# Performance work log

Hardware: AMD Instinct MI355X
Metric: run time of the kernel (lower is better)

The kernel has to match this reference:

```python
import jax, jax.numpy as jnp
import numpy as np

# Network topology constants (topological order: inputs, L hidden layers, outputs)
N_IN = 512
H = 1024      # hidden nodes per layer
L = 8         # hidden layers
N_OUT = 256
DEG = 64      # enabled incoming connections per non-input node
B = 1024      # batch of input vectors

LAYER_SIZES = [H] * L + [N_OUT]
E_TOTAL = sum(n * DEG for n in LAYER_SIZES)  # 540672


def setup_inputs() -> dict:
    key = jax.random.key(0)
    k_in, k_w = jax.random.split(key)
    inputs = jax.random.normal(k_in, (B, N_IN), dtype=jnp.float32)
    # scale weights ~1/sqrt(DEG) so sigmoid pre-activations are well-conditioned
    weights = jax.random.normal(k_w, (E_TOTAL,), dtype=jnp.float32) / np.sqrt(DEG)
    # src indices: for each layer, incoming edges may come from ANY earlier node
    rng = np.random.default_rng(0)
    src_chunks = []
    n_before = N_IN
    for n in LAYER_SIZES:
        src_chunks.append(rng.integers(0, n_before, size=n * DEG))
        n_before += n
    src_idx = jnp.asarray(np.concatenate(src_chunks), dtype=jnp.int32)
    return {"inputs": inputs, "weights": weights, "src_idx": src_idx}


def reference(inputs, weights, src_idx):
    # outs: [B, n_nodes_evaluated_so_far], grown layer by layer (topological order)
    outs = inputs
    off = 0
    for n in LAYER_SIZES:
        e = n * DEG
        s = src_idx[off:off + e]            # [e] gather indices into earlier nodes
        w = weights[off:off + e]            # [e]
        gathered = outs[:, s] * w           # [B, e] irregular gather + scale
        z = gathered.reshape(-1, n, DEG).sum(-1)  # per-node sum over DEG in-edges
        outs = jnp.concatenate([outs, jax.nn.sigmoid(z)], axis=1)
        off += e
    return outs[:, -N_OUT:]  # [B, N_OUT] outputs of 'output' nodes
```

## Files before the change

kernel.cpp:

```cpp
#include <hip/hip_runtime.h>
#include <math.h>


#define N_IN    512
#define NLAYER  9
#define DEG     64
#define BATCH   1024
#define BPB     4
#define THREADS 1024
#define TOTAL_N 8960
#define N_OUT   256
#define NGROUP  132

union H4 { uint2 u; _Float16 h[4]; };
union H2 { unsigned u; _Float16 h[2]; };
union HS { _Float16 h; unsigned short s; };

__global__ __launch_bounds__(256)
void neat_prep(const float* __restrict__ wts,
               const int*   __restrict__ sidx,
               uint4*       __restrict__ rec)
{
    __shared__ unsigned short srec[64 * 17 * 8];

    const int tid  = threadIdx.x;
    const int g    = blockIdx.x;
    const int wave = tid >> 6;
    const int lane = tid & 63;
    const unsigned long long lt = (1ull << lane) - 1ull;

    #pragma unroll 2
    for (int k = 0; k < 16; ++k) {
        const int l = (wave << 4) + k;
        const int j = (g << 12) + (l << 6) + lane;
        const int idx = sidx[j];
        HS w; w.h = (_Float16)wts[j];

        const int c = idx & 15;
        int start = 0, rank = 0;
        #pragma unroll
        for (int cc = 0; cc < 16; ++cc) {
            const unsigned long long m = __ballot(c == cc);
            if (cc < c)       start += (int)__popcll(m);
            else if (cc == c) rank   = (int)__popcll(m & lt);
        }

        const int sigma = ((l & 15) << 2) | (l >> 4);
        const int slot  = ((start + rank) - sigma) & 63;
        const int q = slot >> 2, gg = slot & 3;
        srec[((l * 17 + q) << 3) + gg]     = (unsigned short)idx;
        srec[((l * 17 + q) << 3) + 4 + gg] = w.s;
    }
    __syncthreads();

    const uint4* sr = reinterpret_cast<const uint4*>(srec);
    for (int r = tid; r < 1024; r += 256) {
        const int q = r >> 6, l = r & 63;
        rec[(g << 10) + r] = sr[l * 17 + q];
    }
}

__global__ __launch_bounds__(THREADS, 4)
void neat_fwd(const float* __restrict__ in,
              const uint4* __restrict__ rec,
              float*       __restrict__ out)
{
    __shared__ _Float16 act[TOTAL_N * BPB];

    const int tid   = threadIdx.x;
    const int bbase = blockIdx.x * BPB;

    {
        const float* src = in + bbase * N_IN;
        for (int t = tid; t < BPB * N_IN; t += THREADS) {
            int j = t >> 9;
            int i = t & (N_IN - 1);
            act[i * BPB + j] = (_Float16)src[t];
        }
    }
    __syncthreads();

    int recBase = 0;
    int nb      = N_IN;
    #pragma unroll 1
    for (int layer = 0; layer < NLAYER; ++layer) {
        const int n = (layer < NLAYER - 1) ? 1024 : N_OUT;
        if (tid < n) {
            const int neuron = tid;
            const uint4* rp = rec + recBase + ((neuron >> 6) << 10) + (neuron & 63);

            uint4 r[16];
            #pragma unroll
            for (int q = 0; q < 16; ++q) r[q] = rp[q << 6];

            float4 acc = make_float4(0.f, 0.f, 0.f, 0.f);
            #pragma unroll
            for (int q = 0; q < 16; ++q) {
                const uint4 r4 = r[q];
                H4 g0, g1, g2, g3;
                g0.u = *reinterpret_cast<const uint2*>(act + ((r4.x & 0xffffu) << 2));
                g1.u = *reinterpret_cast<const uint2*>(act + ((r4.x >> 16) << 2));
                g2.u = *reinterpret_cast<const uint2*>(act + ((r4.y & 0xffffu) << 2));
                g3.u = *reinterpret_cast<const uint2*>(act + ((r4.y >> 16) << 2));
                H2 wz, ww; wz.u = r4.z; ww.u = r4.w;
                acc.x += (float)g0.h[0] * (float)wz.h[0];
                acc.y += (float)g0.h[1] * (float)wz.h[0];
                acc.z += (float)g0.h[2] * (float)wz.h[0];
                acc.w += (float)g0.h[3] * (float)wz.h[0];
                acc.x += (float)g1.h[0] * (float)wz.h[1];
                acc.y += (float)g1.h[1] * (float)wz.h[1];
                acc.z += (float)g1.h[2] * (float)wz.h[1];
                acc.w += (float)g1.h[3] * (float)wz.h[1];
                acc.x += (float)g2.h[0] * (float)ww.h[0];
                acc.y += (float)g2.h[1] * (float)ww.h[0];
                acc.z += (float)g2.h[2] * (float)ww.h[0];
                acc.w += (float)g2.h[3] * (float)ww.h[0];
                acc.x += (float)g3.h[0] * (float)ww.h[1];
                acc.y += (float)g3.h[1] * (float)ww.h[1];
                acc.z += (float)g3.h[2] * (float)ww.h[1];
                acc.w += (float)g3.h[3] * (float)ww.h[1];
            }

            float4 sg;
            sg.x = 1.f / (1.f + __expf(-acc.x));
            sg.y = 1.f / (1.f + __expf(-acc.y));
            sg.z = 1.f / (1.f + __expf(-acc.z));
            sg.w = 1.f / (1.f + __expf(-acc.w));

            if (layer < NLAYER - 1) {
                H4 p;
                p.h[0] = (_Float16)sg.x; p.h[1] = (_Float16)sg.y;
                p.h[2] = (_Float16)sg.z; p.h[3] = (_Float16)sg.w;
                *reinterpret_cast<uint2*>(act + ((nb + neuron) << 2)) = p.u;
            } else {
                float* op = out + neuron;
                op[(bbase + 0) * N_OUT] = sg.x;
                op[(bbase + 1) * N_OUT] = sg.y;
                op[(bbase + 2) * N_OUT] = sg.z;
                op[(bbase + 3) * N_OUT] = sg.w;
            }
        }
        __syncthreads();
        recBase += n << 4;
        nb      += n;
    }
}

extern "C" void kernel_launch(void* const* d_in, const int* in_sizes, int n_in,
                              void* d_out, int out_size, void* d_ws, size_t ws_size,
                              hipStream_t stream)
{
    const float* in  = (const float*)d_in[0];
    const float* wts = (const float*)d_in[1];
    const int*   sx  = (const int*)d_in[2];
    float*       out = (float*)d_out;
    uint4*       rec = (uint4*)d_ws;

    neat_prep<<<NGROUP, 256, 0, stream>>>(wts, sx, rec);
    neat_fwd<<<BATCH / BPB, THREADS, 0, stream>>>(in, rec, out);
}
```

Measured before the change: 55.33 us.

## Fuse edge-record prep into forward kernel with a grid-wide barrier

Merges the separate prep kernel into the forward kernel. Every block first builds its share of the per-edge records with a new slot assignment that sorts by index bank and fills overflow into holes, then all blocks wait on a global atomic-flag barrier before running the layer loop. The aim is to remove the second kernel launch and the serial gap between the two kernels, and to spread prep across all 256 blocks. The cost is a hipMemsetAsync on the flag, two __syncthreads per prep iteration, and a spin barrier that only works if all 256 blocks are resident at the same time.

```diff
diff --git a/kernel.cpp b/kernel.cpp
--- a/kernel.cpp
+++ b/kernel.cpp
@@ -10,64 +10,28 @@
 #define THREADS 1024
 #define TOTAL_N 8960
 #define N_OUT   256
-#define NGROUP  132
+#define NEDGE_N 8448
+#define GRID    256
+#define PREPW   (GRID * 16)
 
 union H4 { uint2 u; _Float16 h[4]; };
 union H2 { unsigned u; _Float16 h[2]; };
 union HS { _Float16 h; unsigned short s; };
 
-__global__ __launch_bounds__(256)
-void neat_prep(const float* __restrict__ wts,
-               const int*   __restrict__ sidx,
-               uint4*       __restrict__ rec)
-{
-    __shared__ unsigned short srec[64 * 17 * 8];
-
-    const int tid  = threadIdx.x;
-    const int g    = blockIdx.x;
-    const int wave = tid >> 6;
-    const int lane = tid & 63;
-    const unsigned long long lt = (1ull << lane) - 1ull;
-
-    #pragma unroll 2
-    for (int k = 0; k < 16; ++k) {
-        const int l = (wave << 4) + k;
-        const int j = (g << 12) + (l << 6) + lane;
-        const int idx = sidx[j];
-        HS w; w.h = (_Float16)wts[j];
-
-        const int c = idx & 15;
-        int start = 0, rank = 0;
-        #pragma unroll
-        for (int cc = 0; cc < 16; ++cc) {
-            const unsigned long long m = __ballot(c == cc);
-            if (cc < c)       start += (int)__popcll(m);
-            else if (cc == c) rank   = (int)__popcll(m & lt);
-        }
-
-        const int sigma = ((l & 15) << 2) | (l >> 4);
-        const int slot  = ((start + rank) - sigma) & 63;
-        const int q = slot >> 2, gg = slot & 3;
-        srec[((l * 17 + q) << 3) + gg]     = (unsigned short)idx;
-        srec[((l * 17 + q) << 3) + 4 + gg] = w.s;
-    }
-    __syncthreads();
-
-    const uint4* sr = reinterpret_cast<const uint4*>(srec);
-    for (int r = tid; r < 1024; r += 256) {
-        const int q = r >> 6, l = r & 63;
-        rec[(g << 10) + r] = sr[l * 17 + q];
-    }
-}
-
 __global__ __launch_bounds__(THREADS, 4)
-void neat_fwd(const float* __restrict__ in,
-              const uint4* __restrict__ rec,
-              float*       __restrict__ out)
+void neat_fused(const float* __restrict__ in,
+                const float* __restrict__ wts,
+                const int*   __restrict__ sidx,
+                uint4*       __restrict__ rec,
+                int*         __restrict__ flag,
+                float*       __restrict__ out)
 {
     __shared__ _Float16 act[TOTAL_N * BPB];
+    __shared__ unsigned sortbuf[16][64];
 
     const int tid   = threadIdx.x;
+    const int wave  = tid >> 6;
+    const int lane  = tid & 63;
     const int bbase = blockIdx.x * BPB;
 
     {
@@ -78,7 +42,69 @@
             act[i * BPB + j] = (_Float16)src[t];
         }
     }
+
+    const unsigned long long lt = (1ull << lane) - 1ull;
+    const int wgid = blockIdx.x * 16 + wave;
+    for (int t = wgid; t < NEDGE_N; t += PREPW) {
+        const int e   = (t << 6) + lane;
+        const int idx = sidx[e];
+        HS w; w.h = (_Float16)wts[e];
+        const int c = idx & 15;
+
+        int rank = 0, spillbefore = 0;
+        #pragma unroll
+        for (int cc = 0; cc < 16; ++cc) {
+            const unsigned long long m = __ballot(c == cc);
+            const int n = (int)__popcll(m);
+            if (cc == c) rank = (int)__popcll(m & lt);
+            spillbefore += (cc < c && n > 4) ? (n - 4) : 0;
+        }
+        const bool spill = (rank >= 4);
+        int slot_pre = spill ? -1 : ((c << 2) + rank);
+        const int myspill = spillbefore + rank - 4;
+
+        int hcum = 0;
+        #pragma unroll
+        for (int cc = 0; cc < 16; ++cc) {
+            const unsigned long long m = __ballot(c == cc);
+            const int n = (int)__popcll(m);
+            int holes = 4 - n; holes = holes > 0 ? holes : 0;
+            const bool take = (slot_pre < 0) && (myspill < hcum + holes);
+            slot_pre = take ? ((cc << 2) + n + (myspill - hcum)) : slot_pre;
+            hcum += holes;
+        }
+
+        const int fl    = t & 63;
+        const int sigma = ((fl & 15) << 2) | (fl >> 4);
+        const int slot  = (slot_pre + sigma) & 63;
+        sortbuf[wave][slot] = (unsigned)idx | ((unsigned)w.s << 16);
+        __syncthreads();
+        if (lane < 16) {
+            const unsigned s0 = sortbuf[wave][(lane << 2) + 0];
+            const unsigned s1 = sortbuf[wave][(lane << 2) + 1];
+            const unsigned s2 = sortbuf[wave][(lane << 2) + 2];
+            const unsigned s3 = sortbuf[wave][(lane << 2) + 3];
+            uint4 o;
+            o.x = (s0 & 0xffffu) | (s1 << 16);
+            o.y = (s2 & 0xffffu) | (s3 << 16);
+            o.z = (s0 >> 16) | (s1 & 0xffff0000u);
+            o.w = (s2 >> 16) | (s3 & 0xffff0000u);
+            rec[((t >> 6) << 10) + (lane << 6) + fl] = o;
+        }
+        __syncthreads();
+    }
+
+    __threadfence();
     __syncthreads();
+    if (tid == 0) {
+        atomicAdd(flag, 1);
+        while (__hip_atomic_load(flag, __ATOMIC_ACQUIRE,
+                                 __HIP_MEMORY_SCOPE_AGENT) < GRID) {
+            __builtin_amdgcn_s_sleep(2);
+        }
+    }
+    __syncthreads();
+    __threadfence();
 
     int recBase = 0;
     int nb      = N_IN;
@@ -154,8 +180,10 @@
     const float* wts = (const float*)d_in[1];
     const int*   sx  = (const int*)d_in[2];
     float*       out = (float*)d_out;
-    uint4*       rec = (uint4*)d_ws;
 
-    neat_prep<<<NGROUP, 256, 0, stream>>>(wts, sx, rec);
-    neat_fwd<<<BATCH / BPB, THREADS, 0, stream>>>(in, rec, out);
+    int*   flag = (int*)d_ws;
+    uint4* rec  = (uint4*)((char*)d_ws + 256);
+
+    hipMemsetAsync(d_ws, 0, 256, stream);
+    neat_fused<<<GRID, THREADS, 0, stream>>>(in, wts, sx, rec, flag, out);
 }
```

Result: slower. 198.1 us (+258.1%).
